# Kernel tuning notes

Hardware: AMD Instinct MI355X
Metric: run time of the kernel (lower is better)

Reference implementation:

```python
import jax, jax.numpy as jnp
import numpy as np
from jax import lax

B, IN_CH, OUT_CH, K, STYLE_DIM, H, W = 4, 512, 512, 3, 512, 64, 64


def setup_inputs() -> dict:
    key = jax.random.key(0)
    ks = jax.random.split(key, 6)
    x = jax.random.normal(ks[0], (B, B * IN_CH, H, W), dtype=jnp.float32)
    style = jax.random.normal(ks[1], (B, STYLE_DIM), dtype=jnp.float32)
    # learned params
    weight = jax.random.normal(ks[2], (1, OUT_CH, IN_CH, K, K), dtype=jnp.float32)
    demod = jnp.ones((1, OUT_CH, 1, 1), dtype=jnp.float32)
    # nn.Linear(style_dim, in_channels): kaiming-uniform-ish init approximated
    lim = 1.0 / np.sqrt(STYLE_DIM)
    mod_w = jax.random.uniform(ks[3], (IN_CH, STYLE_DIM), minval=-lim, maxval=lim, dtype=jnp.float32)
    mod_b = jax.random.uniform(ks[4], (IN_CH,), minval=-lim, maxval=lim, dtype=jnp.float32)
    return {"x": x, "style": style, "weight": weight, "demod": demod, "mod_w": mod_w, "mod_b": mod_b}


def reference(x, style, weight, demod, mod_w, mod_b):
    b = x.shape[0]
    out_ch, in_ch, k = weight.shape[1], weight.shape[2], weight.shape[3]
    # style modulation: Linear(style) -> (B, in_ch) -> (B,1,in_ch,1,1)
    s = style @ mod_w.T + mod_b
    w = weight * s[:, None, :, None, None]          # (B, out, in, k, k)
    # demod (1,out,1,1) broadcasts against trailing (in,k,k) axes -> needs out==in (as in torch)
    w = w * demod
    w = w.reshape(b * out_ch, in_ch, k, k)           # OIHW grouped kernel
    pad = k // 2
    out = lax.conv_general_dilated(
        x, w,
        window_strides=(1, 1),
        padding=[(pad, pad), (pad, pad)],
        dimension_numbers=("NCHW", "OIHW", "NCHW"),
        feature_group_count=b,
    )
    return out  # (B, B*out_ch, H, W)
```

## Files before the change

### kernel.cpp

```cpp
#include <hip/hip_runtime.h>

typedef __attribute__((ext_vector_type(4))) float f32x4;
typedef __attribute__((ext_vector_type(8))) short bf16x8;
typedef unsigned long long u64;
typedef unsigned short u16;
typedef unsigned int u32;

static __device__ __forceinline__ u16 f2bf(float f) {
    u32 u = __float_as_uint(f);
    u += 0x7fffu + ((u >> 16) & 1u);
    return (u16)(u >> 16);
}

__global__ void k_style(const float* __restrict__ style, const float* __restrict__ mod_w,
                        const float* __restrict__ mod_b, float* __restrict__ s_ws) {
    int t = blockIdx.x * 256 + threadIdx.x;
    int g = t >> 9, ic = t & 511;
    const f32x4* st = (const f32x4*)(style + (g << 9));
    const f32x4* mw = (const f32x4*)(mod_w + (ic << 9));
    float acc = 0.f;
#pragma unroll 4
    for (int d = 0; d < 128; ++d) {
        f32x4 a = st[d], b = mw[d];
        acc += a[0]*b[0] + a[1]*b[1] + a[2]*b[2] + a[3]*b[3];
    }
    s_ws[t] = acc + mod_b[ic];
}

__global__ void k_wmod(const float* __restrict__ weight, const float* __restrict__ demod,
                       const float* __restrict__ s_ws, short* __restrict__ wmod) {
    int t = blockIdx.x * 256 + threadIdx.x;
    int lane = t & 63; int r = t >> 6;
    int m = r & 3; r >>= 2;
    int ch = r & 15; r >>= 4;
    int wr = r & 1; r >>= 1;
    int ocb = r & 3;
    int oc  = ocb*128 + wr*64 + m*16 + (lane & 15);
    int ic0 = ch*32 + (lane >> 4)*8;
    const float* wp = weight + (size_t)(oc*512 + ic0)*9;
    float wv[8][9];
#pragma unroll
    for (int e = 0; e < 8; ++e)
#pragma unroll
        for (int tp = 0; tp < 9; ++tp) wv[e][tp] = wp[e*9 + tp];
    float dm[8];
#pragma unroll
    for (int e = 0; e < 8; ++e) dm[e] = demod[ic0 + e];
#pragma unroll 1
    for (int g = 0; g < 4; ++g) {
        float sv[8];
#pragma unroll
        for (int e = 0; e < 8; ++e) sv[e] = s_ws[(g << 9) + ic0 + e] * dm[e];
        short* base = wmod + ((size_t)((g*4 + ocb)*2 + wr)) * 294912 + ((size_t)m << 9) + (lane << 3);
#pragma unroll
        for (int tp = 0; tp < 9; ++tp) {
            bf16x8 pk;
#pragma unroll
            for (int e = 0; e < 8; ++e) pk[e] = (short)f2bf(wv[e][tp] * sv[e]);
            *(bf16x8*)&base[(size_t)(ch*9 + tp) << 11] = pk;
        }
    }
}

__global__ __launch_bounds__(256) void k_xcast(const float* __restrict__ x,
                                               short* __restrict__ xb) {
    __shared__ short Ls[64 * 520];
    const int tid = threadIdx.x;
    const int y = blockIdx.x, g = blockIdx.y, nb = blockIdx.z;
    const float* src = x + (((size_t)(nb * 2048 + (g << 9))) << 12) + (y << 6);
#pragma unroll
    for (int it = 0; it < 32; ++it) {
        int j = it * 256 + tid;
        int ic = j >> 4, p4 = j & 15;
        f32x4 v = *(const f32x4*)(src + ((size_t)ic << 12) + (p4 << 2));
        int kk = (ic >> 3) & 3;
        int fb = (ic >> 5) * 32 + (ic & 7);
#pragma unroll
        for (int c = 0; c < 4; ++c) {
            int px = (p4 << 2) + c;
            int k = kk ^ ((px >> 1) & 3);
            Ls[px * 520 + fb + k * 8] = (short)f2bf(v[c]);
        }
    }
    __syncthreads();
    short* dstb = xb + ((size_t)((nb * 4 + g) * 64 + y) << 15);
#pragma unroll
    for (int it = 0; it < 16; ++it) {
        int j = it * 256 + tid;
        int ch = j >> 8, px = (j >> 2) & 63, k = j & 3;
        *(bf16x8*)&dstb[(size_t)j << 3] = *(const bf16x8*)&Ls[px * 520 + ch * 32 + k * 8];
    }
}

__global__ __launch_bounds__(256, 3) void k_conv(const short* __restrict__ xb,
                                                 const short* __restrict__ wmod,
                                                 float* __restrict__ out) {
    __shared__ __align__(16) short Xs[2 * 8448];

    const int tid  = threadIdx.x;
    const int lane = tid & 63;
    const int wv   = tid >> 6;
    const int wr   = wv >> 1, wc = wv & 1;
    const int l15  = lane & 15;
    const int l4   = lane >> 4;
    const int ocb  = blockIdx.x & 3, rowb = blockIdx.x >> 2;
    const int g    = blockIdx.y, nb = blockIdx.z;
    const int y0   = rowb << 1;

    const short* xbg = xb + ((size_t)((nb * 4 + g) * 64) << 15);
    const short* wg  = wmod + ((size_t)((g * 4 + ocb) * 2 + wr)) * 294912;
    float* outg = out + (((size_t)(nb * 2048 + (g << 9) + ocb * 128)) << 12) + (rowb << 7);

    const int gy = y0 - 1 + wv;
    const bool srow = (gy >= 0 && gy <= 63);
    const short* xsrc = xbg + ((size_t)(srow ? gy : 0) << 15) + (lane << 3);
    short* xdst0 = Xs + ((wv * 66 + 1) << 5);

    const short* wp   = wg + (lane << 3);
    const short* wend = wg + 143 * 2048 + (lane << 3);

    for (int i = tid; i < 4224; i += 256) ((u64*)Xs)[i] = 0ull;

    f32x4 acc[4][4];
#pragma unroll
    for (int m = 0; m < 4; ++m)
#pragma unroll
        for (int nn = 0; nn < 4; ++nn) acc[m][nn] = (f32x4){0.f, 0.f, 0.f, 0.f};

    __syncthreads();

    if (srow) {
#pragma unroll
        for (int q = 0; q < 4; ++q)
            __builtin_amdgcn_global_load_lds(
                (const __attribute__((address_space(1))) void*)(xsrc + (q << 9)),
                (__attribute__((address_space(3))) void*)(xdst0 + (q << 9)), 16, 0, 0);
    }
    __builtin_amdgcn_sched_barrier(0);
    bf16x8 na0 = *(const bf16x8*)(wp);
    bf16x8 na1 = *(const bf16x8*)(wp + 512);
    bf16x8 na2 = *(const bf16x8*)(wp + 1024);
    bf16x8 na3 = *(const bf16x8*)(wp + 1536);
    wp += 2048;

#pragma unroll 1
    for (int ch = 0; ch < 16; ++ch) {
        asm volatile("s_waitcnt vmcnt(4)" ::: "memory");
        __builtin_amdgcn_s_barrier();
        __builtin_amdgcn_sched_barrier(0);
        if (ch < 15 && srow) {
            const short* s = xsrc + ((size_t)(ch + 1) << 11);
            short* d = xdst0 + (((ch + 1) & 1) ? 8448 : 0);
#pragma unroll
            for (int q = 0; q < 4; ++q)
                __builtin_amdgcn_global_load_lds(
                    (const __attribute__((address_space(1))) void*)(s + (q << 9)),
                    (__attribute__((address_space(3))) void*)(d + (q << 9)), 16, 0, 0);
        }
        __builtin_amdgcn_sched_barrier(0);
        const int bb = (ch & 1) * 8448;

#pragma unroll
        for (int tap = 0; tap < 9; ++tap) {
            const int dy = tap / 3 - 1, dx = tap % 3 - 1;
            bf16x8 ca0 = na0, ca1 = na1, ca2 = na2, ca3 = na3;
            na0 = *(const bf16x8*)(wp);
            na1 = *(const bf16x8*)(wp + 512);
            na2 = *(const bf16x8*)(wp + 1024);
            na3 = *(const bf16x8*)(wp + 1536);
            wp = (wp < wend) ? (wp + 2048) : wp;

            const int bofs = bb + (((wc + 1 + dy) * 66 + 1 + dx + l15) << 5)
                           + ((l4 ^ (((l15 + dx) >> 1) & 3)) << 3);
            bf16x8 b0 = *(const bf16x8*)&Xs[bofs];
            bf16x8 b1 = *(const bf16x8*)&Xs[bofs + 512];
            bf16x8 b2 = *(const bf16x8*)&Xs[bofs + 1024];
            bf16x8 b3 = *(const bf16x8*)&Xs[bofs + 1536];

            __builtin_amdgcn_s_setprio(1);
            acc[0][0] = __builtin_amdgcn_mfma_f32_16x16x32_bf16(ca0, b0, acc[0][0], 0, 0, 0);
            acc[1][0] = __builtin_amdgcn_mfma_f32_16x16x32_bf16(ca1, b0, acc[1][0], 0, 0, 0);
            acc[2][0] = __builtin_amdgcn_mfma_f32_16x16x32_bf16(ca2, b0, acc[2][0], 0, 0, 0);
            acc[3][0] = __builtin_amdgcn_mfma_f32_16x16x32_bf16(ca3, b0, acc[3][0], 0, 0, 0);
            acc[0][1] = __builtin_amdgcn_mfma_f32_16x16x32_bf16(ca0, b1, acc[0][1], 0, 0, 0);
            acc[1][1] = __builtin_amdgcn_mfma_f32_16x16x32_bf16(ca1, b1, acc[1][1], 0, 0, 0);
            acc[2][1] = __builtin_amdgcn_mfma_f32_16x16x32_bf16(ca2, b1, acc[2][1], 0, 0, 0);
            acc[3][1] = __builtin_amdgcn_mfma_f32_16x16x32_bf16(ca3, b1, acc[3][1], 0, 0, 0);
            acc[0][2] = __builtin_amdgcn_mfma_f32_16x16x32_bf16(ca0, b2, acc[0][2], 0, 0, 0);
            acc[1][2] = __builtin_amdgcn_mfma_f32_16x16x32_bf16(ca1, b2, acc[1][2], 0, 0, 0);
            acc[2][2] = __builtin_amdgcn_mfma_f32_16x16x32_bf16(ca2, b2, acc[2][2], 0, 0, 0);
            acc[3][2] = __builtin_amdgcn_mfma_f32_16x16x32_bf16(ca3, b2, acc[3][2], 0, 0, 0);
            acc[0][3] = __builtin_amdgcn_mfma_f32_16x16x32_bf16(ca0, b3, acc[0][3], 0, 0, 0);
            acc[1][3] = __builtin_amdgcn_mfma_f32_16x16x32_bf16(ca1, b3, acc[1][3], 0, 0, 0);
            acc[2][3] = __builtin_amdgcn_mfma_f32_16x16x32_bf16(ca2, b3, acc[2][3], 0, 0, 0);
            acc[3][3] = __builtin_amdgcn_mfma_f32_16x16x32_bf16(ca3, b3, acc[3][3], 0, 0, 0);
            __builtin_amdgcn_s_setprio(0);
        }
    }

#pragma unroll
    for (int m = 0; m < 4; ++m)
#pragma unroll
        for (int nn = 0; nn < 4; ++nn) {
            const int oc = (wr << 6) + (m << 4) + (l4 << 2);
            const int p  = (wc << 6) + (nn << 4) + l15;
            float* dst = outg + ((size_t)oc << 12) + p;
#pragma unroll
            for (int r = 0; r < 4; ++r) dst[(size_t)r << 12] = acc[m][nn][r];
        }
}

extern "C" void kernel_launch(void* const* d_in, const int* in_sizes, int n_in,
                              void* d_out, int out_size, void* d_ws, size_t ws_size,
                              hipStream_t stream) {
    const float* x      = (const float*)d_in[0];
    const float* style  = (const float*)d_in[1];
    const float* weight = (const float*)d_in[2];
    const float* demod  = (const float*)d_in[3];
    const float* mod_w  = (const float*)d_in[4];
    const float* mod_b  = (const float*)d_in[5];
    float* out = (float*)d_out;

    float* s_ws = (float*)d_ws;
    short* wmod = (short*)((char*)d_ws + 8192);
    short* xbuf = (short*)((char*)d_ws + 8192 + 18874368);

    hipLaunchKernelGGL(k_style, dim3(8), dim3(256), 0, stream, style, mod_w, mod_b, s_ws);
    hipLaunchKernelGGL(k_wmod, dim3(128), dim3(256), 0, stream, weight, demod, s_ws, wmod);
    hipLaunchKernelGGL(k_xcast, dim3(64, 4, 4), dim3(256), 0, stream, x, xbuf);
    hipLaunchKernelGGL(k_conv, dim3(128, 4, 4), dim3(256), 0, stream, xbuf, wmod, out);
}
```

Measured before the change: 313.5 us.

## Switch conv inner product to 32x32x16 MFMA with matching weight layout

The convolution kernel now uses 32x32x16 bf16 MFMA tiles instead of 16x16x32, with 2x2 f32x16 accumulators per wave. The weight-packing kernel and the LDS B-operand addressing are reworked to match the new lane mapping, and tap offsets are precomputed once per channel chunk. The end-of-buffer clamp on the weight prefetch pointer is removed, and the occupancy hint goes from 3 to 4 blocks. The aim is fewer MFMA issues and simpler address arithmetic per tap. In exchange, the higher occupancy target may force register spills, and the final prefetch now reads past the per-group weight slice.

```diff
diff --git a/kernel.cpp b/kernel.cpp
--- a/kernel.cpp
+++ b/kernel.cpp
@@ -1,6 +1,7 @@
 #include <hip/hip_runtime.h>
 
 typedef __attribute__((ext_vector_type(4))) float f32x4;
+typedef __attribute__((ext_vector_type(16))) float f32x16;
 typedef __attribute__((ext_vector_type(8))) short bf16x8;
 typedef unsigned long long u64;
 typedef unsigned short u16;
@@ -31,12 +32,13 @@
                        const float* __restrict__ s_ws, short* __restrict__ wmod) {
     int t = blockIdx.x * 256 + threadIdx.x;
     int lane = t & 63; int r = t >> 6;
-    int m = r & 3; r >>= 2;
+    int oh = r & 1; r >>= 1;
+    int kk = r & 1; r >>= 1;
     int ch = r & 15; r >>= 4;
     int wr = r & 1; r >>= 1;
     int ocb = r & 3;
-    int oc  = ocb*128 + wr*64 + m*16 + (lane & 15);
-    int ic0 = ch*32 + (lane >> 4)*8;
+    int oc  = ocb*128 + wr*64 + oh*32 + (lane & 31);
+    int ic0 = ch*32 + kk*16 + (lane >> 5)*8;
     const float* wp = weight + (size_t)(oc*512 + ic0)*9;
     float wv[8][9];
 #pragma unroll
@@ -51,7 +53,8 @@
         float sv[8];
 #pragma unroll
         for (int e = 0; e < 8; ++e) sv[e] = s_ws[(g << 9) + ic0 + e] * dm[e];
-        short* base = wmod + ((size_t)((g*4 + ocb)*2 + wr)) * 294912 + ((size_t)m << 9) + (lane << 3);
+        short* base = wmod + ((size_t)((g*4 + ocb)*2 + wr)) * 294912
+                    + (((kk << 1) + oh) << 9) + (lane << 3);
 #pragma unroll
         for (int tp = 0; tp < 9; ++tp) {
             bf16x8 pk;
@@ -92,7 +95,7 @@
     }
 }
 
-__global__ __launch_bounds__(256, 3) void k_conv(const short* __restrict__ xb,
+__global__ __launch_bounds__(256, 4) void k_conv(const short* __restrict__ xb,
                                                  const short* __restrict__ wmod,
                                                  float* __restrict__ out) {
     __shared__ __align__(16) short Xs[2 * 8448];
@@ -101,8 +104,8 @@
     const int lane = tid & 63;
     const int wv   = tid >> 6;
     const int wr   = wv >> 1, wc = wv & 1;
-    const int l15  = lane & 15;
-    const int l4   = lane >> 4;
+    const int l31  = lane & 31;
+    const int lh   = lane >> 5;
     const int ocb  = blockIdx.x & 3, rowb = blockIdx.x >> 2;
     const int g    = blockIdx.y, nb = blockIdx.z;
     const int y0   = rowb << 1;
@@ -116,16 +119,17 @@
     const short* xsrc = xbg + ((size_t)(srow ? gy : 0) << 15) + (lane << 3);
     short* xdst0 = Xs + ((wv * 66 + 1) << 5);
 
-    const short* wp   = wg + (lane << 3);
-    const short* wend = wg + 143 * 2048 + (lane << 3);
+    const short* wp = wg + (lane << 3);
 
     for (int i = tid; i < 4224; i += 256) ((u64*)Xs)[i] = 0ull;
 
-    f32x4 acc[4][4];
-#pragma unroll
-    for (int m = 0; m < 4; ++m)
-#pragma unroll
-        for (int nn = 0; nn < 4; ++nn) acc[m][nn] = (f32x4){0.f, 0.f, 0.f, 0.f};
+    f32x16 acc[2][2];
+#pragma unroll
+    for (int oh = 0; oh < 2; ++oh)
+#pragma unroll
+        for (int ph = 0; ph < 2; ++ph)
+#pragma unroll
+            for (int r = 0; r < 16; ++r) acc[oh][ph][r] = 0.f;
 
     __syncthreads();
 
@@ -160,53 +164,51 @@
         __builtin_amdgcn_sched_barrier(0);
         const int bb = (ch & 1) * 8448;
 
+        int pB[3];
+#pragma unroll
+        for (int d = 0; d < 3; ++d) {
+            const int xr = l31 + d - 1;
+            pB[d] = bb + ((wc * 66 + 1 + xr) << 5) + ((lh ^ ((xr >> 1) & 3)) << 3);
+        }
+
 #pragma unroll
         for (int tap = 0; tap < 9; ++tap) {
-            const int dy = tap / 3 - 1, dx = tap % 3 - 1;
             bf16x8 ca0 = na0, ca1 = na1, ca2 = na2, ca3 = na3;
             na0 = *(const bf16x8*)(wp);
             na1 = *(const bf16x8*)(wp + 512);
             na2 = *(const bf16x8*)(wp + 1024);
             na3 = *(const bf16x8*)(wp + 1536);
-            wp = (wp < wend) ? (wp + 2048) : wp;
-
-            const int bofs = bb + (((wc + 1 + dy) * 66 + 1 + dx + l15) << 5)
-                           + ((l4 ^ (((l15 + dx) >> 1) & 3)) << 3);
-            bf16x8 b0 = *(const bf16x8*)&Xs[bofs];
-            bf16x8 b1 = *(const bf16x8*)&Xs[bofs + 512];
-            bf16x8 b2 = *(const bf16x8*)&Xs[bofs + 1024];
-            bf16x8 b3 = *(const bf16x8*)&Xs[bofs + 1536];
+            wp += 2048;
+
+            const int p0 = pB[tap % 3] + (tap / 3) * 2112;
+            const int p1 = p0 ^ 16;
+            bf16x8 b00 = *(const bf16x8*)&Xs[p0];
+            bf16x8 b01 = *(const bf16x8*)&Xs[p0 + 1024];
+            bf16x8 b10 = *(const bf16x8*)&Xs[p1];
+            bf16x8 b11 = *(const bf16x8*)&Xs[p1 + 1024];
 
             __builtin_amdgcn_s_setprio(1);
-            acc[0][0] = __builtin_amdgcn_mfma_f32_16x16x32_bf16(ca0, b0, acc[0][0], 0, 0, 0);
-            acc[1][0] = __builtin_amdgcn_mfma_f32_16x16x32_bf16(ca1, b0, acc[1][0], 0, 0, 0);
-            acc[2][0] = __builtin_amdgcn_mfma_f32_16x16x32_bf16(ca2, b0, acc[2][0], 0, 0, 0);
-            acc[3][0] = __builtin_amdgcn_mfma_f32_16x16x32_bf16(ca3, b0, acc[3][0], 0, 0, 0);
-            acc[0][1] = __builtin_amdgcn_mfma_f32_16x16x32_bf16(ca0, b1, acc[0][1], 0, 0, 0);
-            acc[1][1] = __builtin_amdgcn_mfma_f32_16x16x32_bf16(ca1, b1, acc[1][1], 0, 0, 0);
-            acc[2][1] = __builtin_amdgcn_mfma_f32_16x16x32_bf16(ca2, b1, acc[2][1], 0, 0, 0);
-            acc[3][1] = __builtin_amdgcn_mfma_f32_16x16x32_bf16(ca3, b1, acc[3][1], 0, 0, 0);
-            acc[0][2] = __builtin_amdgcn_mfma_f32_16x16x32_bf16(ca0, b2, acc[0][2], 0, 0, 0);
-            acc[1][2] = __builtin_amdgcn_mfma_f32_16x16x32_bf16(ca1, b2, acc[1][2], 0, 0, 0);
-            acc[2][2] = __builtin_amdgcn_mfma_f32_16x16x32_bf16(ca2, b2, acc[2][2], 0, 0, 0);
-            acc[3][2] = __builtin_amdgcn_mfma_f32_16x16x32_bf16(ca3, b2, acc[3][2], 0, 0, 0);
-            acc[0][3] = __builtin_amdgcn_mfma_f32_16x16x32_bf16(ca0, b3, acc[0][3], 0, 0, 0);
-            acc[1][3] = __builtin_amdgcn_mfma_f32_16x16x32_bf16(ca1, b3, acc[1][3], 0, 0, 0);
-            acc[2][3] = __builtin_amdgcn_mfma_f32_16x16x32_bf16(ca2, b3, acc[2][3], 0, 0, 0);
-            acc[3][3] = __builtin_amdgcn_mfma_f32_16x16x32_bf16(ca3, b3, acc[3][3], 0, 0, 0);
+            acc[0][0] = __builtin_amdgcn_mfma_f32_32x32x16_bf16(ca0, b00, acc[0][0], 0, 0, 0);
+            acc[0][1] = __builtin_amdgcn_mfma_f32_32x32x16_bf16(ca0, b01, acc[0][1], 0, 0, 0);
+            acc[1][0] = __builtin_amdgcn_mfma_f32_32x32x16_bf16(ca1, b00, acc[1][0], 0, 0, 0);
+            acc[1][1] = __builtin_amdgcn_mfma_f32_32x32x16_bf16(ca1, b01, acc[1][1], 0, 0, 0);
+            acc[0][0] = __builtin_amdgcn_mfma_f32_32x32x16_bf16(ca2, b10, acc[0][0], 0, 0, 0);
+            acc[0][1] = __builtin_amdgcn_mfma_f32_32x32x16_bf16(ca2, b11, acc[0][1], 0, 0, 0);
+            acc[1][0] = __builtin_amdgcn_mfma_f32_32x32x16_bf16(ca3, b10, acc[1][0], 0, 0, 0);
+            acc[1][1] = __builtin_amdgcn_mfma_f32_32x32x16_bf16(ca3, b11, acc[1][1], 0, 0, 0);
             __builtin_amdgcn_s_setprio(0);
         }
     }
 
 #pragma unroll
-    for (int m = 0; m < 4; ++m)
-#pragma unroll
-        for (int nn = 0; nn < 4; ++nn) {
-            const int oc = (wr << 6) + (m << 4) + (l4 << 2);
-            const int p  = (wc << 6) + (nn << 4) + l15;
-            float* dst = outg + ((size_t)oc << 12) + p;
-#pragma unroll
-            for (int r = 0; r < 4; ++r) dst[(size_t)r << 12] = acc[m][nn][r];
+    for (int oh = 0; oh < 2; ++oh)
+#pragma unroll
+        for (int ph = 0; ph < 2; ++ph) {
+            float* dst = outg + ((size_t)((wr << 6) + (oh << 5) + (lh << 2)) << 12)
+                       + (wc << 6) + (ph << 5) + l31;
+#pragma unroll
+            for (int r = 0; r < 16; ++r)
+                dst[(size_t)(((r & 3) + ((r >> 2) << 3)) << 12)] = acc[oh][ph][r];
         }
 }
 
```

Result: slower. 370.6 us (+18.2%).

## Deepen weight prefetch in conv, precompute LDS offsets, parallelize wmod over groups

Applied to the files above, without the earlier changes.

The conv kernel now keeps two taps of weight fragments in flight instead of one. The wait count is raised to match, and the end-of-buffer clamp is dropped, so the last taps read a little past the group's weight slab. The LDS tap offsets are precomputed once per channel chunk as three base offsets plus a row stride, which cuts per-tap integer work. k_wmod launches four times as many blocks with one group per thread, trading repeated weight loads for more parallelism. The extra prefetch stage adds register pressure and out-of-range reads that are never used.

```diff
diff --git a/kernel.cpp b/kernel.cpp
--- a/kernel.cpp
+++ b/kernel.cpp
@@ -34,31 +34,21 @@
     int m = r & 3; r >>= 2;
     int ch = r & 15; r >>= 4;
     int wr = r & 1; r >>= 1;
-    int ocb = r & 3;
+    int ocb = r & 3; r >>= 2;
+    int g = r & 3;
     int oc  = ocb*128 + wr*64 + m*16 + (lane & 15);
     int ic0 = ch*32 + (lane >> 4)*8;
     const float* wp = weight + (size_t)(oc*512 + ic0)*9;
-    float wv[8][9];
-#pragma unroll
-    for (int e = 0; e < 8; ++e)
-#pragma unroll
-        for (int tp = 0; tp < 9; ++tp) wv[e][tp] = wp[e*9 + tp];
-    float dm[8];
-#pragma unroll
-    for (int e = 0; e < 8; ++e) dm[e] = demod[ic0 + e];
-#pragma unroll 1
-    for (int g = 0; g < 4; ++g) {
-        float sv[8];
-#pragma unroll
-        for (int e = 0; e < 8; ++e) sv[e] = s_ws[(g << 9) + ic0 + e] * dm[e];
-        short* base = wmod + ((size_t)((g*4 + ocb)*2 + wr)) * 294912 + ((size_t)m << 9) + (lane << 3);
-#pragma unroll
-        for (int tp = 0; tp < 9; ++tp) {
-            bf16x8 pk;
-#pragma unroll
-            for (int e = 0; e < 8; ++e) pk[e] = (short)f2bf(wv[e][tp] * sv[e]);
-            *(bf16x8*)&base[(size_t)(ch*9 + tp) << 11] = pk;
-        }
+    float sv[8];
+#pragma unroll
+    for (int e = 0; e < 8; ++e) sv[e] = s_ws[(g << 9) + ic0 + e] * demod[ic0 + e];
+    short* base = wmod + ((size_t)((g*4 + ocb)*2 + wr)) * 294912 + ((size_t)m << 9) + (lane << 3);
+#pragma unroll
+    for (int tp = 0; tp < 9; ++tp) {
+        bf16x8 pk;
+#pragma unroll
+        for (int e = 0; e < 8; ++e) pk[e] = (short)f2bf(wp[e*9 + tp] * sv[e]);
+        *(bf16x8*)&base[(size_t)(ch*9 + tp) << 11] = pk;
     }
 }
 
@@ -116,8 +106,7 @@
     const short* xsrc = xbg + ((size_t)(srow ? gy : 0) << 15) + (lane << 3);
     short* xdst0 = Xs + ((wv * 66 + 1) << 5);
 
-    const short* wp   = wg + (lane << 3);
-    const short* wend = wg + 143 * 2048 + (lane << 3);
+    const short* wp = wg + (lane << 3);
 
     for (int i = tid; i < 4224; i += 256) ((u64*)Xs)[i] = 0ull;
 
@@ -137,15 +126,19 @@
                 (__attribute__((address_space(3))) void*)(xdst0 + (q << 9)), 16, 0, 0);
     }
     __builtin_amdgcn_sched_barrier(0);
-    bf16x8 na0 = *(const bf16x8*)(wp);
-    bf16x8 na1 = *(const bf16x8*)(wp + 512);
-    bf16x8 na2 = *(const bf16x8*)(wp + 1024);
-    bf16x8 na3 = *(const bf16x8*)(wp + 1536);
-    wp += 2048;
+    bf16x8 pa0 = *(const bf16x8*)(wp);
+    bf16x8 pa1 = *(const bf16x8*)(wp + 512);
+    bf16x8 pa2 = *(const bf16x8*)(wp + 1024);
+    bf16x8 pa3 = *(const bf16x8*)(wp + 1536);
+    bf16x8 na0 = *(const bf16x8*)(wp + 2048);
+    bf16x8 na1 = *(const bf16x8*)(wp + 2560);
+    bf16x8 na2 = *(const bf16x8*)(wp + 3072);
+    bf16x8 na3 = *(const bf16x8*)(wp + 3584);
+    wp += 4096;
 
 #pragma unroll 1
     for (int ch = 0; ch < 16; ++ch) {
-        asm volatile("s_waitcnt vmcnt(4)" ::: "memory");
+        asm volatile("s_waitcnt vmcnt(8)" ::: "memory");
         __builtin_amdgcn_s_barrier();
         __builtin_amdgcn_sched_barrier(0);
         if (ch < 15 && srow) {
@@ -160,22 +153,29 @@
         __builtin_amdgcn_sched_barrier(0);
         const int bb = (ch & 1) * 8448;
 
+        int pB[3];
+#pragma unroll
+        for (int d = 0; d < 3; ++d) {
+            const int dx = d - 1;
+            pB[d] = bb + ((wc * 66 + 1 + dx + l15) << 5)
+                  + ((l4 ^ (((l15 + dx) >> 1) & 3)) << 3);
+        }
+
 #pragma unroll
         for (int tap = 0; tap < 9; ++tap) {
-            const int dy = tap / 3 - 1, dx = tap % 3 - 1;
-            bf16x8 ca0 = na0, ca1 = na1, ca2 = na2, ca3 = na3;
+            bf16x8 ca0 = pa0, ca1 = pa1, ca2 = pa2, ca3 = pa3;
+            pa0 = na0; pa1 = na1; pa2 = na2; pa3 = na3;
             na0 = *(const bf16x8*)(wp);
             na1 = *(const bf16x8*)(wp + 512);
             na2 = *(const bf16x8*)(wp + 1024);
             na3 = *(const bf16x8*)(wp + 1536);
-            wp = (wp < wend) ? (wp + 2048) : wp;
-
-            const int bofs = bb + (((wc + 1 + dy) * 66 + 1 + dx + l15) << 5)
-                           + ((l4 ^ (((l15 + dx) >> 1) & 3)) << 3);
-            bf16x8 b0 = *(const bf16x8*)&Xs[bofs];
-            bf16x8 b1 = *(const bf16x8*)&Xs[bofs + 512];
-            bf16x8 b2 = *(const bf16x8*)&Xs[bofs + 1024];
-            bf16x8 b3 = *(const bf16x8*)&Xs[bofs + 1536];
+            wp += 2048;
+
+            const int p0 = pB[tap % 3] + (tap / 3) * 2112;
+            bf16x8 b0 = *(const bf16x8*)&Xs[p0];
+            bf16x8 b1 = *(const bf16x8*)&Xs[p0 + 512];
+            bf16x8 b2 = *(const bf16x8*)&Xs[p0 + 1024];
+            bf16x8 b3 = *(const bf16x8*)&Xs[p0 + 1536];
 
             __builtin_amdgcn_s_setprio(1);
             acc[0][0] = __builtin_amdgcn_mfma_f32_16x16x32_bf16(ca0, b0, acc[0][0], 0, 0, 0);
@@ -226,7 +226,7 @@
     short* xbuf = (short*)((char*)d_ws + 8192 + 18874368);
 
     hipLaunchKernelGGL(k_style, dim3(8), dim3(256), 0, stream, style, mod_w, mod_b, s_ws);
-    hipLaunchKernelGGL(k_wmod, dim3(128), dim3(256), 0, stream, weight, demod, s_ws, wmod);
+    hipLaunchKernelGGL(k_wmod, dim3(512), dim3(256), 0, stream, weight, demod, s_ws, wmod);
     hipLaunchKernelGGL(k_xcast, dim3(64, 4, 4), dim3(256), 0, stream, x, xbuf);
     hipLaunchKernelGGL(k_conv, dim3(128, 4, 4), dim3(256), 0, stream, xbuf, wmod, out);
 }
```

After: 310.9 us. No clear change (-0.8%).
